# Kernel tuning notes

Hardware: AMD Instinct MI355X
Metric: run time of the kernel (lower is better)

Reference implementation:

```python
import jax, jax.numpy as jnp
import numpy as np

# Static configuration (matches init_kwargs)
B, C, H, W = 8, 64, 256, 256
WS = 8            # window size
HEADS = 4
DH = 16           # dim per head, HEADS*DH == C
L = WS * WS       # tokens per window
EPS_LN = 1e-5

# --- Swin relative-position index (static, numpy) ---
_coords = np.stack(np.meshgrid(np.arange(WS), np.arange(WS), indexing='ij'))  # [2,ws,ws]
_flat = _coords.reshape(2, -1)                                                # [2,L]
_rel = (_flat[:, :, None] - _flat[:, None, :]).transpose(1, 2, 0).copy()      # [L,L,2]
_rel[..., 0] += WS - 1
_rel[..., 1] += WS - 1
_rel[..., 0] *= 2 * WS - 1
REL_IDX = _rel.sum(-1)  # [L,L] ints in [0, (2ws-1)^2)


def _biasfree_ln(x, w):
    # x: [B,C,H,W]; BiasFree_LayerNorm over channel dim (biased var, no mean subtraction in scale)
    var = jnp.var(x, axis=1, keepdims=True)
    return x * jax.lax.rsqrt(var + EPS_LN) * w[None, :, None, None]


def _win_partition(t):  # [B,H,W,C] -> [N, L, C]
    t = t.reshape(B, H // WS, WS, W // WS, WS, C).transpose(0, 1, 3, 2, 4, 5)
    return t.reshape(-1, L, C)


def _win_reverse(t):  # [N, L, C] -> [B,H,W,C]
    t = t.reshape(B, H // WS, W // WS, WS, WS, C).transpose(0, 1, 3, 2, 4, 5)
    return t.reshape(B, H, W, C)


def _l2norm(t):
    # torch F.normalize(dim=-1) semantics
    n = jnp.sqrt(jnp.sum(t * t, axis=-1, keepdims=True))
    return t / jnp.maximum(n, 1e-12)


def _forward(x, illu_fea, ln1_w, ln2_w, w_qkv, b_qkv, rpb_table, w_proj, b_proj,
             temperature, w_qkv_m, w_dw, w_out_m):
    # ---------- spatial (window) attention branch ----------
    xs = _biasfree_ln(x, ln1_w).transpose(0, 2, 3, 1)          # [B,H,W,C]
    xw = _win_partition(xs)                                     # [N,L,C]
    iw = _win_partition(illu_fea.transpose(0, 2, 3, 1))         # [N,L,C]
    iw = iw.reshape(-1, L, HEADS, DH).transpose(0, 2, 1, 3)     # [N,h,L,d]

    qkv = (xw @ w_qkv + b_qkv).reshape(-1, L, 3, HEADS, DH).transpose(2, 0, 3, 1, 4)
    q, k, v = qkv[0], qkv[1], qkv[2]                            # [N,h,L,d]
    scale = DH ** (-0.5)
    attn = jnp.einsum('nhld,nhmd->nhlm', q * scale, k)          # [N,h,L,L]
    bias = rpb_table[REL_IDX.reshape(-1)].reshape(L, L, HEADS).transpose(2, 0, 1)
    attn = jax.nn.softmax(attn + bias[None], axis=-1)
    v = v * iw                                                  # illumination modulation
    out = jnp.einsum('nhlm,nhmd->nhld', attn, v)
    out = out.transpose(0, 2, 1, 3).reshape(-1, L, C) @ w_proj + b_proj
    win_out = _win_reverse(out).transpose(0, 3, 1, 2)           # [B,C,H,W]

    # ---------- channel (MDTA) attention branch ----------
    xm = _biasfree_ln(x, ln2_w)
    qkv_m = jnp.einsum('oc,bchw->bohw', w_qkv_m, xm)            # 1x1 conv, [B,3C,H,W]
    qkv_m = jax.lax.conv_general_dilated(
        qkv_m, w_dw, (1, 1), 'SAME', feature_group_count=3 * C,
        dimension_numbers=('NCHW', 'OIHW', 'NCHW'))             # depthwise 3x3
    qm, km, vm = jnp.split(qkv_m, 3, axis=1)                    # [B,C,H,W] each

    def heads(t):
        return t.reshape(B, HEADS, DH, H * W)                   # b (n d) h w -> b n d (hw)
    qm, km, vm, im = heads(qm), heads(km), heads(vm), heads(illu_fea)
    qm = _l2norm(qm)
    km = _l2norm(km)
    attn_c = jnp.einsum('bndx,bnex->bnde', qm, km) * temperature[None]  # [B,h,d,d]
    attn_c = jax.nn.softmax(attn_c, axis=-1)
    vm = vm * im                                                # illumination modulation
    out_c = jnp.einsum('bnde,bnex->bndx', attn_c, vm).reshape(B, C, H, W)
    mdta_out = jnp.einsum('oc,bchw->bohw', w_out_m, out_c)

    return x + win_out + mdta_out


def setup_inputs() -> dict:
    key = jax.random.key(0)
    ks = jax.random.split(key, 10)
    f32 = jnp.float32
    return {
        'x': jax.random.normal(ks[0], (B, C, H, W), f32),
        'illu_fea': jax.random.uniform(ks[1], (B, C, H, W), f32),
        'ln1_w': jnp.ones((C,), f32),
        'ln2_w': jnp.ones((C,), f32),
        'w_qkv': jax.random.normal(ks[2], (C, 3 * C), f32) * 0.02,
        'b_qkv': jnp.zeros((3 * C,), f32),
        'rpb_table': jax.random.normal(ks[3], ((2 * WS - 1) ** 2, HEADS), f32) * 0.02,
        'w_proj': jax.random.normal(ks[4], (C, C), f32) * 0.02,
        'b_proj': jnp.zeros((C,), f32),
        'temperature': jnp.ones((HEADS, 1, 1), f32),
        'w_qkv_m': jax.random.normal(ks[5], (3 * C, C), f32) * 0.02,
        'w_dw': jax.random.normal(ks[6], (3 * C, 1, 3, 3), f32) * 0.1,
        'w_out_m': jax.random.normal(ks[7], (C, C), f32) * 0.02,
    }


def reference(x, illu_fea, ln1_w, ln2_w, w_qkv, b_qkv, rpb_table, w_proj, b_proj,
              temperature, w_qkv_m, w_dw, w_out_m):
    return _forward(x, illu_fea, ln1_w, ln2_w, w_qkv, b_qkv, rpb_table, w_proj,
                    b_proj, temperature, w_qkv_m, w_dw, w_out_m)
```

## Files before the change

### kernel.cpp

```cpp
#include <hip/hip_runtime.h>
#include <hip/hip_bf16.h>

#define HW 65536
#define WIDTH 256
#define SP_OFF 77856768ull

typedef __attribute__((ext_vector_type(8))) short short8v;
typedef __attribute__((ext_vector_type(4))) short short4v;
typedef __attribute__((ext_vector_type(4))) float f32x4;

__device__ inline float bf2f(unsigned short u) {
  unsigned int i = ((unsigned int)u) << 16;
  float f; __builtin_memcpy(&f, &i, 4); return f;
}
__device__ inline unsigned short f2bf(float x) {
  __hip_bfloat16 h = __float2bfloat16(x);
  unsigned short u; __builtin_memcpy(&u, &h, 2); return u;
}

#define XH_IDX(p, g) ((p)*64 + ((((g) ^ ((p)&7)))<<3))
#define QC_IDX(ch, px) ((ch)*256 + ((((px)>>3) ^ ((ch)&7))<<3) + ((px)&7))
#define QCG_IDX(ch, G) ((ch)*256 + ((((G) ^ ((ch)&7)))<<3))

__global__ __launch_bounds__(256, 3) void k_spatial(
    const float* __restrict__ x, const float* __restrict__ illu,
    const float* __restrict__ ln1w, const float* __restrict__ wqkv,
    const float* __restrict__ bqkv, const float* __restrict__ rpb,
    const float* __restrict__ wproj, const float* __restrict__ bproj,
    float* __restrict__ out, unsigned short* __restrict__ sp, int use_sp)
{
  __shared__ __align__(16) unsigned short shbuf[9216];
  __shared__ __align__(16) unsigned short ks[64*72];
  __shared__ __align__(16) unsigned short vs[64*72];
  __shared__ __align__(16) unsigned short vsT[64*72];
  __shared__ float rpbs[900];
  __shared__ float rs_tok[64];

  unsigned short* xw = shbuf;
  unsigned short* qs = shbuf + 4608;

  const int tid = threadIdx.x;
  const int b = blockIdx.x & 7;
  const int grp = blockIdx.x >> 3;
  const float* xb = x + (size_t)b * 64 * HW;
  const float* ib = illu + (size_t)b * 64 * HW;

  const int lane = tid & 63;
  const int w = tid >> 6;
  const int fr = lane & 15;
  const int fg = lane >> 4;
  const int hb = w * 16;

  for (int i = tid; i < 900; i += 256) rpbs[i] = rpb[i];

  short8v bfq[3][2];
  float biasr[3];
  #pragma unroll
  for (int part = 0; part < 3; ++part) {
    int o = part * 64 + hb + fr;
    biasr[part] = bqkv[o];
    #pragma unroll
    for (int kh = 0; kh < 2; ++kh)
      #pragma unroll
      for (int j = 0; j < 8; ++j) {
        int c = kh * 32 + fg * 8 + j;
        bfq[part][kh][j] = (short)f2bf(wqkv[c * 192 + o] * ln1w[c]);
      }
  }
  short8v bfp[2];
  #pragma unroll
  for (int kh = 0; kh < 2; ++kh)
    #pragma unroll
    for (int j = 0; j < 8; ++j) {
      int c = kh * 32 + fg * 8 + j;
      bfp[kh][j] = (short)f2bf(wproj[c * 64 + hb + fr]);
    }

  for (int wi = 0; wi < 4; ++wi) {
    const int win = (grp << 2) + wi;
    const int h0 = (win >> 5) << 3;
    const int w0 = (win & 31) << 3;

    for (int i = tid; i < 1024; i += 256) {
      int c = i >> 4, seg = i & 15;
      int row = seg >> 1, half = (seg & 1) * 4;
      float4 v4 = *(const float4*)&xb[(size_t)c * HW + (h0 + row) * WIDTH + w0 + half];
      int p = row * 8 + half;
      xw[(p+0)*72 + c] = f2bf(v4.x);
      xw[(p+1)*72 + c] = f2bf(v4.y);
      xw[(p+2)*72 + c] = f2bf(v4.z);
      xw[(p+3)*72 + c] = f2bf(v4.w);
    }
    __syncthreads();
    {
      int l = tid >> 2, q4 = tid & 3;
      short8v v8a = *(const short8v*)&xw[l*72 + q4*16];
      short8v v8b = *(const short8v*)&xw[l*72 + q4*16 + 8];
      float s = 0.f, s2 = 0.f;
      #pragma unroll
      for (int j = 0; j < 8; ++j) {
        float va = bf2f((unsigned short)v8a[j]), vb = bf2f((unsigned short)v8b[j]);
        s += va + vb; s2 += va * va + vb * vb;
      }
      s += __shfl_down(s, 1); s2 += __shfl_down(s2, 1);
      s += __shfl_down(s, 2); s2 += __shfl_down(s2, 2);
      if (q4 == 0) {
        float mean = s * 0.015625f;
        float var = s2 * 0.015625f - mean * mean;
        rs_tok[l] = rsqrtf(var + 1e-5f);
      }
    }
    __syncthreads();
    {
      short8v a[4][2];
      #pragma unroll
      for (int rt = 0; rt < 4; ++rt)
        #pragma unroll
        for (int kh = 0; kh < 2; ++kh)
          a[rt][kh] = *(const short8v*)&xw[(rt*16 + fr)*72 + kh*32 + fg*8];
      #pragma unroll
      for (int part = 0; part < 3; ++part) {
        float bias = biasr[part];
        #pragma unroll
        for (int rt = 0; rt < 4; ++rt) {
          f32x4 acc = {0.f, 0.f, 0.f, 0.f};
          acc = __builtin_amdgcn_mfma_f32_16x16x32_bf16(a[rt][0], bfq[part][0], acc, 0, 0, 0);
          acc = __builtin_amdgcn_mfma_f32_16x16x32_bf16(a[rt][1], bfq[part][1], acc, 0, 0, 0);
          #pragma unroll
          for (int r = 0; r < 4; ++r) {
            int t = rt*16 + fg*4 + r;
            float val = acc[r] * rs_tok[t] + bias;
            if (part == 0)      qs[t*72 + hb + fr] = f2bf(val * 0.25f);
            else if (part == 1) ks[t*72 + hb + fr] = f2bf(val);
            else                vs[t*72 + hb + fr] = f2bf(val);
          }
        }
      }
    }
    __syncthreads();
    for (int i = tid; i < 1024; i += 256) {
      int c = i >> 4, seg = i & 15;
      int row = seg >> 1, half = (seg & 1) * 4;
      float4 v4 = *(const float4*)&ib[(size_t)c * HW + (h0 + row) * WIDTH + w0 + half];
      int p = row * 8 + half;
      xw[(p+0)*72 + c] = f2bf(v4.x);
      xw[(p+1)*72 + c] = f2bf(v4.y);
      xw[(p+2)*72 + c] = f2bf(v4.z);
      xw[(p+3)*72 + c] = f2bf(v4.w);
    }
    __syncthreads();
    for (int i = tid; i < 4096; i += 256) {
      int l = i >> 6, c = i & 63;
      unsigned short vb16 = f2bf(bf2f(vs[l*72 + c]) * bf2f(xw[l*72 + c]));
      vs[l*72 + c] = vb16;
      vsT[c*72 + ((((l >> 3) ^ (c & 7)) << 3) | (l & 7))] = vb16;
    }
    __syncthreads();
    float inv_s[4];
    {
      short8v zero8 = {0,0,0,0,0,0,0,0};
      short8v kf[4], qf[4];
      #pragma unroll
      for (int t = 0; t < 4; ++t) {
        if (fg < 2) {
          kf[t] = *(const short8v*)&ks[(t*16 + fr)*72 + hb + fg*8];
          qf[t] = *(const short8v*)&qs[(t*16 + fr)*72 + hb + fg*8];
        } else { kf[t] = zero8; qf[t] = zero8; }
      }
      f32x4 st[4][4];
      #pragma unroll
      for (int kt = 0; kt < 4; ++kt)
        #pragma unroll
        for (int qt = 0; qt < 4; ++qt) {
          f32x4 z = {0.f, 0.f, 0.f, 0.f};
          st[kt][qt] = __builtin_amdgcn_mfma_f32_16x16x32_bf16(kf[kt], qf[qt], z, 0, 0, 0);
        }
      float sc[4][16];
      #pragma unroll
      for (int qt = 0; qt < 4; ++qt) {
        int qi = qt*2 + (fr >> 3);
        int qj = fr & 7;
        float mx = -1e30f;
        #pragma unroll
        for (int kt = 0; kt < 4; ++kt) {
          int ki = kt*2 + (fg >> 1);
          int kj0 = (fg & 1) * 4;
          int base = ((qi - ki + 7)*15 + (qj - kj0 + 7))*4 + w;
          #pragma unroll
          for (int r = 0; r < 4; ++r) {
            float v = st[kt][qt][r] + rpbs[base - 4*r];
            sc[qt][kt*4 + r] = v;
            mx = fmaxf(mx, v);
          }
        }
        mx = fmaxf(mx, __shfl_xor(mx, 16));
        mx = fmaxf(mx, __shfl_xor(mx, 32));
        float ss = 0.f;
        #pragma unroll
        for (int j = 0; j < 16; ++j) { float e = __expf(sc[qt][j] - mx); sc[qt][j] = e; ss += e; }
        ss += __shfl_xor(ss, 16);
        ss += __shfl_xor(ss, 32);
        inv_s[qt] = 1.f / ss;
      }
      __syncthreads();
      unsigned short* pb = shbuf + w * 2304;
      f32x4 ot[4];
      #pragma unroll
      for (int nt = 0; nt < 4; ++nt) { f32x4 z = {0.f,0.f,0.f,0.f}; ot[nt] = z; }
      #pragma unroll
      for (int P = 0; P < 2; ++P) {
        #pragma unroll
        for (int qt = 0; qt < 4; ++qt)
          #pragma unroll
          for (int k2 = 0; k2 < 2; ++k2) {
            int kt = 2*P + k2;
            unsigned int lo = (unsigned)f2bf(sc[qt][kt*4+0]) | ((unsigned)f2bf(sc[qt][kt*4+1]) << 16);
            unsigned int hi = (unsigned)f2bf(sc[qt][kt*4+2]) | ((unsigned)f2bf(sc[qt][kt*4+3]) << 16);
            uint2 pk; pk.x = lo; pk.y = hi;
            *(uint2*)&pb[(qt*16 + fr)*36 + k2*16 + fg*4] = pk;
          }
        __syncthreads();
        short8v av = *(const short8v*)&vsT[(hb + fr)*72 + (((P*4 + fg) ^ ((hb + fr) & 7)) << 3)];
        #pragma unroll
        for (int nt = 0; nt < 4; ++nt) {
          short4v p0 = *(const short4v*)&pb[(nt*16 + fr)*36 + fg*8];
          short4v p1 = *(const short4v*)&pb[(nt*16 + fr)*36 + fg*8 + 4];
          short8v bv;
          #pragma unroll
          for (int j = 0; j < 4; ++j) { bv[j] = p0[j]; bv[4+j] = p1[j]; }
          ot[nt] = __builtin_amdgcn_mfma_f32_16x16x32_bf16(av, bv, ot[nt], 0, 0, 0);
        }
        __syncthreads();
      }
      #pragma unroll
      for (int nt = 0; nt < 4; ++nt) {
        float iv = inv_s[nt];
        unsigned int lo = (unsigned)f2bf(ot[nt][0]*iv) | ((unsigned)f2bf(ot[nt][1]*iv) << 16);
        unsigned int hi = (unsigned)f2bf(ot[nt][2]*iv) | ((unsigned)f2bf(ot[nt][3]*iv) << 16);
        uint2 pk; pk.x = lo; pk.y = hi;
        *(uint2*)&ks[(nt*16 + fr)*72 + hb + fg*4] = pk;
      }
    }
    __syncthreads();
    {
      short8v a[4][2];
      #pragma unroll
      for (int rt = 0; rt < 4; ++rt)
        #pragma unroll
        for (int kh = 0; kh < 2; ++kh)
          a[rt][kh] = *(const short8v*)&ks[(rt*16 + fr)*72 + kh*32 + fg*8];
      #pragma unroll
      for (int rt = 0; rt < 4; ++rt) {
        f32x4 acc = {0.f, 0.f, 0.f, 0.f};
        acc = __builtin_amdgcn_mfma_f32_16x16x32_bf16(a[rt][0], bfp[0], acc, 0, 0, 0);
        acc = __builtin_amdgcn_mfma_f32_16x16x32_bf16(a[rt][1], bfp[1], acc, 0, 0, 0);
        #pragma unroll
        for (int r = 0; r < 4; ++r)
          vs[(rt*16 + fg*4 + r)*72 + hb + fr] = f2bf(acc[r]);
      }
    }
    __syncthreads();
    if (use_sp) {
      unsigned short* spw = sp + (size_t)(b * 1024 + win) * 4096;
      for (int i = tid; i < 1024; i += 256) {
        int row = i >> 7, rem = i & 127;
        int c = rem >> 1, half = (rem & 1) * 4;
        int p = row * 8 + half;
        size_t gofs = (size_t)c * HW + (h0 + row) * WIDTH + w0 + half;
        float4 xr4 = *(const float4*)&xb[gofs];
        float bp = bproj[c];
        unsigned int lo = (unsigned)f2bf(xr4.x + bp + bf2f(vs[(p+0)*72 + c]))
                        | ((unsigned)f2bf(xr4.y + bp + bf2f(vs[(p+1)*72 + c])) << 16);
        unsigned int hi = (unsigned)f2bf(xr4.z + bp + bf2f(vs[(p+2)*72 + c]))
                        | ((unsigned)f2bf(xr4.w + bp + bf2f(vs[(p+3)*72 + c])) << 16);
        uint2 pk; pk.x = lo; pk.y = hi;
        *(uint2*)&spw[row*512 + c*8 + half] = pk;
      }
    } else {
      for (int i = tid; i < 1024; i += 256) {
        int o = i >> 4, seg = i & 15;
        int row = seg >> 1, half = (seg & 1) * 4;
        int p = row * 8 + half;
        size_t gofs = (size_t)o * HW + (h0 + row) * WIDTH + w0 + half;
        float4 xr4 = *(const float4*)&xb[gofs];
        float bp = bproj[o];
        float4 r;
        r.x = xr4.x + bp + bf2f(vs[(p+0)*72 + o]);
        r.y = xr4.y + bp + bf2f(vs[(p+1)*72 + o]);
        r.z = xr4.z + bp + bf2f(vs[(p+2)*72 + o]);
        r.w = xr4.w + bp + bf2f(vs[(p+3)*72 + o]);
        *(float4*)&out[(size_t)b * 64 * HW + gofs] = r;
      }
    }
    __syncthreads();
  }
}

__global__ __launch_bounds__(256, 2) void k_chan_qkv(
    const float* __restrict__ x, const float* __restrict__ illu,
    const float* __restrict__ ln2w, const float* __restrict__ w1,
    const float* __restrict__ wdw,
    unsigned short* __restrict__ vm, float* __restrict__ Gp,
    float* __restrict__ Nqp, float* __restrict__ Nkp)
{
  __shared__ __align__(16) unsigned short xh[324*64];
  __shared__ __align__(16) unsigned short tb[32*360];
  __shared__ __align__(16) unsigned short qc[16*256];
  __shared__ __align__(16) unsigned short kc[16*256];

  float* rsp = (float*)tb;

  const int tid = threadIdx.x;
  const int blk = ((blockIdx.x & 7) << 8) | (blockIdx.x >> 3);
  const int b = blk >> 8;
  const int tile = blk & 255;
  const int ty0 = (tile >> 4) << 4, tx0 = (tile & 15) << 4;
  const float* xb = x + (size_t)b * 64 * HW;

  for (int i = tid; i < 64 * 324; i += 256) {
    int c = i / 324, p = i - c * 324;
    int hy = p / 18, hx = p - hy * 18;
    int gy = ty0 + hy - 1, gx = tx0 + hx - 1;
    float v = 0.f;
    if (gy >= 0 && gy < 256 && gx >= 0 && gx < 256)
      v = xb[(size_t)c * HW + gy * WIDTH + gx];
    xh[XH_IDX(p, c >> 3) + (c & 7)] = f2bf(v);
  }
  __syncthreads();
  for (int p = tid; p < 324; p += 256) {
    float s = 0.f, s2 = 0.f;
    #pragma unroll
    for (int g = 0; g < 8; ++g) {
      short8v v8 = *(const short8v*)&xh[XH_IDX(p, g)];
      #pragma unroll
      for (int j = 0; j < 8; ++j) { float v = bf2f((unsigned short)v8[j]); s += v; s2 += v * v; }
    }
    float mean = s * 0.015625f;
    float var = s2 * 0.015625f - mean * mean;
    rsp[p] = rsqrtf(var + 1e-5f);
  }
  __syncthreads();
  for (int i = tid; i < 2592; i += 256) {
    int p = i >> 3;
    float rs = rsp[p];
    short8v v8 = *(const short8v*)&xh[i * 8];
    #pragma unroll
    for (int j = 0; j < 8; ++j) v8[j] = (short)f2bf(bf2f((unsigned short)v8[j]) * rs);
    *(short8v*)&xh[i * 8] = v8;
  }
  __syncthreads();

  const int lane = tid & 63;
  const int wid = tid >> 6;
  const int fcol = lane & 15;
  const int fk = lane >> 4;
  const int dpy = (tid >> 2) & 15;
  const int dg = tid & 3;

  auto gemm32 = [&](int qb, int kb) {
    short8v bq[2], bk[2];
    const float* wrq = w1 + (size_t)(qb + fcol) * 64;
    const float* wrk = w1 + (size_t)(kb + fcol) * 64;
    #pragma unroll
    for (int s = 0; s < 2; ++s) {
      int cs = fk * 8 + s * 32;
      #pragma unroll
      for (int j = 0; j < 8; ++j) {
        float lw = ln2w[cs + j];
        bq[s][j] = (short)f2bf(wrq[cs + j] * lw);
        bk[s][j] = (short)f2bf(wrk[cs + j] * lw);
      }
    }
    for (int t = wid; t < 21; t += 4) {
      int ar = t * 16 + fcol;
      short8v a0, a1;
      if (ar < 324) {
        a0 = *(const short8v*)&xh[XH_IDX(ar, fk)];
        a1 = *(const short8v*)&xh[XH_IDX(ar, fk + 4)];
      } else {
        short8v z = {0,0,0,0,0,0,0,0};
        a0 = z; a1 = z;
      }
      f32x4 aq = {0.f, 0.f, 0.f, 0.f};
      f32x4 ak = {0.f, 0.f, 0.f, 0.f};
      aq = __builtin_amdgcn_mfma_f32_16x16x32_bf16(a0, bq[0], aq, 0, 0, 0);
      aq = __builtin_amdgcn_mfma_f32_16x16x32_bf16(a1, bq[1], aq, 0, 0, 0);
      ak = __builtin_amdgcn_mfma_f32_16x16x32_bf16(a0, bk[0], ak, 0, 0, 0);
      ak = __builtin_amdgcn_mfma_f32_16x16x32_bf16(a1, bk[1], ak, 0, 0, 0);
      #pragma unroll
      for (int r = 0; r < 4; ++r) {
        int px = t * 16 + fk * 4 + r;
        if (px < 324) {
          int hy = px / 18, hx = px - hy * 18;
          tb[fcol * 360 + hy * 20 + hx]        = f2bf(aq[r]);
          tb[(16 + fcol) * 360 + hy * 20 + hx] = f2bf(ak[r]);
        }
      }
    }
  };

  float dout8[8][4];
  auto dw32 = [&](int qwb, int kwb) {
    #pragma unroll
    for (int oc8 = 0; oc8 < 8; ++oc8) {
      int oc = wid * 8 + oc8;
      int ch = (oc < 16) ? (qwb + oc) : (kwb + oc - 16);
      const float* w9 = wdw + (size_t)ch * 9;
      float wk[9];
      #pragma unroll
      for (int t = 0; t < 9; ++t) wk[t] = w9[t];
      float a0 = 0.f, a1 = 0.f, a2 = 0.f, a3 = 0.f;
      #pragma unroll
      for (int ky = 0; ky < 3; ++ky) {
        int base = oc * 360 + (dpy + ky) * 20 + dg * 4;
        short4v t4 = *(const short4v*)&tb[base];
        unsigned int t2 = *(const unsigned int*)&tb[base + 4];
        float e0 = bf2f((unsigned short)t4[0]);
        float e1 = bf2f((unsigned short)t4[1]);
        float e2 = bf2f((unsigned short)t4[2]);
        float e3 = bf2f((unsigned short)t4[3]);
        float e4 = bf2f((unsigned short)(t2 & 0xffff));
        float e5 = bf2f((unsigned short)(t2 >> 16));
        float k0 = wk[ky*3+0], k1 = wk[ky*3+1], k2 = wk[ky*3+2];
        a0 += k0*e0 + k1*e1 + k2*e2;
        a1 += k0*e1 + k1*e2 + k2*e3;
        a2 += k0*e2 + k1*e3 + k2*e4;
        a3 += k0*e3 + k1*e4 + k2*e5;
      }
      dout8[oc8][0] = a0; dout8[oc8][1] = a1;
      dout8[oc8][2] = a2; dout8[oc8][3] = a3;
    }
  };

  for (int n = 0; n < 4; ++n) {
    gemm32(16 * n, 64 + 16 * n);
    __syncthreads();
    dw32(16 * n, 64 + 16 * n);
    #pragma unroll
    for (int oc8 = 0; oc8 < 8; ++oc8) {
      int oc = wid * 8 + oc8;
      unsigned short* dst = (oc < 16) ? qc : kc;
      int row = oc & 15;
      #pragma unroll
      for (int i = 0; i < 4; ++i)
        dst[QC_IDX(row, dpy*16 + dg*4 + i)] = f2bf(dout8[oc8][i]);
    }
    __syncthreads();
    {
      int ch = tid >> 4, seg = tid & 15;
      float sq = 0.f, sk = 0.f;
      #pragma unroll
      for (int j = 0; j < 16; ++j) {
        float vq = bf2f(qc[QC_IDX(ch, seg * 16 + j)]); sq += vq * vq;
        float vk = bf2f(kc[QC_IDX(ch, seg * 16 + j)]); sk += vk * vk;
      }
      sq += __shfl_xor(sq, 1); sq += __shfl_xor(sq, 2); sq += __shfl_xor(sq, 4); sq += __shfl_xor(sq, 8);
      sk += __shfl_xor(sk, 1); sk += __shfl_xor(sk, 2); sk += __shfl_xor(sk, 4); sk += __shfl_xor(sk, 8);
      if (seg == 0) {
        Nqp[(size_t)blk * 64 + n * 16 + ch] = sq;
        Nkp[(size_t)blk * 64 + n * 16 + ch] = sk;
      }
    }
    if (wid == 0) {
      f32x4 g = {0.f, 0.f, 0.f, 0.f};
      #pragma unroll
      for (int s = 0; s < 8; ++s) {
        int G = fk + 4 * s;
        short8v aq = *(const short8v*)&qc[QCG_IDX(fcol, G)];
        short8v bk = *(const short8v*)&kc[QCG_IDX(fcol, G)];
        g = __builtin_amdgcn_mfma_f32_16x16x32_bf16(aq, bk, g, 0, 0, 0);
      }
      float* gp = Gp + ((size_t)blk * 4 + n) * 256;
      #pragma unroll
      for (int r = 0; r < 4; ++r) gp[(fk * 4 + r) * 16 + fcol] = g[r];
    }
  }
  const float* ib = illu + (size_t)b * 64 * HW;
  for (int j = 0; j < 2; ++j) {
    gemm32(128 + 32 * j, 144 + 32 * j);
    __syncthreads();
    dw32(128 + 32 * j, 144 + 32 * j);
    int gy = ty0 + dpy, gx = tx0 + dg * 4;
    size_t ppos = (size_t)gy * WIDTH + gx;
    #pragma unroll
    for (int oc8 = 0; oc8 < 8; ++oc8) {
      int vc = 32 * j + wid * 8 + oc8;
      float4 iv4 = *(const float4*)&ib[(size_t)vc * HW + ppos];
      unsigned int lo = (unsigned)f2bf(dout8[oc8][0] * iv4.x)
                      | ((unsigned)f2bf(dout8[oc8][1] * iv4.y) << 16);
      unsigned int hi = (unsigned)f2bf(dout8[oc8][2] * iv4.z)
                      | ((unsigned)f2bf(dout8[oc8][3] * iv4.w) << 16);
      uint2 pk; pk.x = lo; pk.y = hi;
      *(uint2*)&vm[((size_t)b * 64 + vc) * HW + ppos] = pk;
    }
    __syncthreads();
  }
}

__global__ __launch_bounds__(256) void k_reduce1(
    const float* __restrict__ Gp, const float* __restrict__ Nqp, const float* __restrict__ Nkp,
    float* __restrict__ G2, float* __restrict__ Nq2, float* __restrict__ Nk2)
{
  const int blk = blockIdx.x;
  const int b = blk >> 5, g = blk & 31;
  const int tid = threadIdx.x;
  float ga[4] = {0.f, 0.f, 0.f, 0.f};
  for (int t = 0; t < 8; ++t) {
    const float* src = Gp + ((size_t)(b * 256 + g * 8 + t)) * 1024;
    #pragma unroll
    for (int j = 0; j < 4; ++j) ga[j] += src[tid + j * 256];
  }
  float* dst = G2 + ((size_t)(b * 32 + g)) * 1024;
  #pragma unroll
  for (int j = 0; j < 4; ++j) dst[tid + j * 256] = ga[j];
  if (tid < 128) {
    int ch = tid & 63; bool isq = tid < 64;
    const float* np = isq ? Nqp : Nkp;
    float s = 0.f;
    for (int t = 0; t < 8; ++t) s += np[((size_t)(b * 256 + g * 8 + t)) * 64 + ch];
    (isq ? Nq2 : Nk2)[(size_t)(b * 32 + g) * 64 + ch] = s;
  }
}

__global__ __launch_bounds__(256) void k_reduce2(
    const float* __restrict__ G2, const float* __restrict__ Nq2, const float* __restrict__ Nk2,
    const float* __restrict__ temp, const float* __restrict__ wout, float* __restrict__ M)
{
  __shared__ float Gs[1024];
  __shared__ float As[4][16][17];
  __shared__ float nq[64], nk[64];
  const int b = blockIdx.x;
  const int tid = threadIdx.x;
  float ga[4] = {0.f, 0.f, 0.f, 0.f};
  for (int g = 0; g < 32; ++g) {
    const float* src = G2 + ((size_t)(b * 32 + g)) * 1024;
    #pragma unroll
    for (int j = 0; j < 4; ++j) ga[j] += src[tid + j * 256];
  }
  #pragma unroll
  for (int j = 0; j < 4; ++j) Gs[tid + j * 256] = ga[j];
  if (tid < 128) {
    int ch = tid & 63; bool isq = tid < 64;
    const float* n2 = isq ? Nq2 : Nk2;
    float s = 0.f;
    for (int g = 0; g < 32; ++g) s += n2[(size_t)(b * 32 + g) * 64 + ch];
    float r = fmaxf(sqrtf(s), 1e-12f);
    (isq ? nq : nk)[ch] = r;
  }
  __syncthreads();
  if (tid < 64) {
    int n = tid >> 4, d = tid & 15;
    float tv = temp[n];
    float row[16]; float mx = -1e30f;
    #pragma unroll
    for (int e = 0; e < 16; ++e) {
      float v = Gs[n * 256 + d * 16 + e] / (nq[n * 16 + d] * nk[n * 16 + e]) * tv;
      row[e] = v; mx = fmaxf(mx, v);
    }
    float s = 0.f;
    #pragma unroll
    for (int e = 0; e < 16; ++e) { float ev = __expf(row[e] - mx); row[e] = ev; s += ev; }
    float inv = 1.f / s;
    #pragma unroll
    for (int e = 0; e < 16; ++e) As[n][d][e] = row[e] * inv;
  }
  __syncthreads();
  float* Mb = M + (size_t)b * 4096;
  for (int i = tid; i < 4096; i += 256) {
    int o = i >> 6, cp = i & 63;
    int n = cp >> 4, e = cp & 15;
    float a = 0.f;
    #pragma unroll
    for (int d = 0; d < 16; ++d) a += wout[o * 64 + n * 16 + d] * As[n][d][e];
    Mb[i] = a;
  }
}

__global__ __launch_bounds__(256, 3) void k_mdta_out(
    const unsigned short* __restrict__ vm, const float* __restrict__ M,
    const unsigned short* __restrict__ sp, int use_sp,
    float* __restrict__ out)
{
  __shared__ __align__(16) float Ml[4096];
  __shared__ __align__(16) unsigned short spl[64 * 264];
  const int blk = blockIdx.x;
  const int b = blk >> 8;
  const int y = blk & 255;
  const int tid = threadIdx.x;

  const float* Mb = M + (size_t)b * 4096;
  for (int i = tid; i < 4096; i += 256) Ml[i] = Mb[i];
  if (use_sp) {
    int wy = y >> 3, py = y & 7;
    const unsigned short* spb = sp + ((((size_t)b * 1024 + wy * 32) * 8) + py) * 512;
    for (int k = 0; k < 8; ++k) {
      int i3 = k * 256 + tid;
      int o = i3 & 63, wx = i3 >> 6;
      short8v v8 = *(const short8v*)&spb[(size_t)wx * 4096 + o * 8];
      *(short8v*)&spl[o * 264 + wx * 8] = v8;
    }
  }
  __syncthreads();
  float xcol[64];
  const unsigned short* vb = vm + (size_t)b * 64 * HW + y * 256 + tid;
  #pragma unroll
  for (int c = 0; c < 64; ++c) xcol[c] = bf2f(vb[(size_t)c * HW]);
  float* ob = out + (size_t)b * 64 * HW + y * 256 + tid;
  for (int o = 0; o < 64; ++o) {
    const float4* mr = (const float4*)&Ml[o * 64];
    float acc = 0.f;
    #pragma unroll
    for (int g = 0; g < 16; ++g) {
      float4 m4 = mr[g];
      acc += m4.x * xcol[g*4] + m4.y * xcol[g*4+1] + m4.z * xcol[g*4+2] + m4.w * xcol[g*4+3];
    }
    if (use_sp) ob[(size_t)o * HW] = bf2f(spl[o * 264 + tid]) + acc;
    else        ob[(size_t)o * HW] += acc;
  }
}

extern "C" void kernel_launch(void* const* d_in, const int* in_sizes, int n_in,
                              void* d_out, int out_size, void* d_ws, size_t ws_size,
                              hipStream_t stream) {
  const float* x     = (const float*)d_in[0];
  const float* illu  = (const float*)d_in[1];
  const float* ln1w  = (const float*)d_in[2];
  const float* ln2w  = (const float*)d_in[3];
  const float* wqkv  = (const float*)d_in[4];
  const float* bqkv  = (const float*)d_in[5];
  const float* rpb   = (const float*)d_in[6];
  const float* wproj = (const float*)d_in[7];
  const float* bproj = (const float*)d_in[8];
  const float* temp  = (const float*)d_in[9];
  const float* w1    = (const float*)d_in[10];
  const float* wdw   = (const float*)d_in[11];
  const float* wout  = (const float*)d_in[12];
  float* out = (float*)d_out;

  char* ws = (char*)d_ws;
  unsigned short* vm = (unsigned short*)ws;
  float* Gp  = (float*)(ws + 67108864);
  float* Nqp = (float*)(ws + 75497472);
  float* Nkp = (float*)(ws + 76021760);
  float* G2  = (float*)(ws + 76546048);
  float* Nq2 = (float*)(ws + 77594624);
  float* Nk2 = (float*)(ws + 77660160);
  float* M   = (float*)(ws + 77725696);
  unsigned short* sp = (unsigned short*)(ws + SP_OFF);
  int use_sp = (ws_size >= SP_OFF + 67108864ull) ? 1 : 0;

  k_spatial<<<2048, 256, 0, stream>>>(x, illu, ln1w, wqkv, bqkv, rpb, wproj, bproj,
                                      out, sp, use_sp);
  k_chan_qkv<<<2048, 256, 0, stream>>>(x, illu, ln2w, w1, wdw, vm, Gp, Nqp, Nkp);
  k_reduce1<<<256, 256, 0, stream>>>(Gp, Nqp, Nkp, G2, Nq2, Nk2);
  k_reduce2<<<8, 256, 0, stream>>>(G2, Nq2, Nk2, temp, wout, M);
  k_mdta_out<<<2048, 256, 0, stream>>>(vm, M, sp, use_sp, out);
}
```

Before: 725.2 us.

## Merge spatial and channel-QKV kernels into one launch with interleaved blocks

Folds the spatial window-attention kernel and the channel QKV/depthwise kernel into a single kernel, with even blocks running the spatial body and odd blocks the channel body over one shared-memory buffer. Both branches read the same x/illu tiles at about the same time, so the goal is cache sharing, overlap of two different workloads on the CUs, and one fewer launch and tail. The cost is that every block reserves the larger shared-memory footprint (about 79KB) and the spatial work drops to two blocks per CU from three, which lowers its occupancy.

```diff
diff --git a/kernel.cpp b/kernel.cpp
--- a/kernel.cpp
+++ b/kernel.cpp
@@ -22,26 +22,27 @@
 #define QC_IDX(ch, px) ((ch)*256 + ((((px)>>3) ^ ((ch)&7))<<3) + ((px)&7))
 #define QCG_IDX(ch, G) ((ch)*256 + ((((G) ^ ((ch)&7)))<<3))
 
-__global__ __launch_bounds__(256, 3) void k_spatial(
+__device__ __forceinline__ void spatial_body(
+    unsigned char* smem, int sub,
     const float* __restrict__ x, const float* __restrict__ illu,
     const float* __restrict__ ln1w, const float* __restrict__ wqkv,
     const float* __restrict__ bqkv, const float* __restrict__ rpb,
     const float* __restrict__ wproj, const float* __restrict__ bproj,
     float* __restrict__ out, unsigned short* __restrict__ sp, int use_sp)
 {
-  __shared__ __align__(16) unsigned short shbuf[9216];
-  __shared__ __align__(16) unsigned short ks[64*72];
-  __shared__ __align__(16) unsigned short vs[64*72];
-  __shared__ __align__(16) unsigned short vsT[64*72];
-  __shared__ float rpbs[900];
-  __shared__ float rs_tok[64];
+  unsigned short* shbuf = (unsigned short*)smem;
+  unsigned short* ks    = (unsigned short*)(smem + 18432);
+  unsigned short* vs    = (unsigned short*)(smem + 27648);
+  unsigned short* vsT   = (unsigned short*)(smem + 36864);
+  float* rpbs           = (float*)(smem + 46080);
+  float* rs_tok         = (float*)(smem + 49680);
 
   unsigned short* xw = shbuf;
   unsigned short* qs = shbuf + 4608;
 
   const int tid = threadIdx.x;
-  const int b = blockIdx.x & 7;
-  const int grp = blockIdx.x >> 3;
+  const int b = sub & 7;
+  const int grp = sub >> 3;
   const float* xb = x + (size_t)b * 64 * HW;
   const float* ib = illu + (size_t)b * 64 * HW;
 
@@ -296,22 +297,22 @@
   }
 }
 
-__global__ __launch_bounds__(256, 2) void k_chan_qkv(
+__device__ __forceinline__ void chan_body(
+    unsigned char* smem, int sub,
     const float* __restrict__ x, const float* __restrict__ illu,
     const float* __restrict__ ln2w, const float* __restrict__ w1,
     const float* __restrict__ wdw,
     unsigned short* __restrict__ vm, float* __restrict__ Gp,
     float* __restrict__ Nqp, float* __restrict__ Nkp)
 {
-  __shared__ __align__(16) unsigned short xh[324*64];
-  __shared__ __align__(16) unsigned short tb[32*360];
-  __shared__ __align__(16) unsigned short qc[16*256];
-  __shared__ __align__(16) unsigned short kc[16*256];
-
+  unsigned short* xh = (unsigned short*)smem;
+  unsigned short* tb = (unsigned short*)(smem + 41472);
+  unsigned short* qc = (unsigned short*)(smem + 64512);
+  unsigned short* kc = (unsigned short*)(smem + 72704);
   float* rsp = (float*)tb;
 
   const int tid = threadIdx.x;
-  const int blk = ((blockIdx.x & 7) << 8) | (blockIdx.x >> 3);
+  const int blk = ((sub & 7) << 8) | (sub >> 3);
   const int b = blk >> 8;
   const int tile = blk & 255;
   const int ty0 = (tile >> 4) << 4, tx0 = (tile & 15) << 4;
@@ -495,6 +496,25 @@
     }
     __syncthreads();
   }
+}
+
+__global__ __launch_bounds__(256, 2) void k_fused(
+    const float* __restrict__ x, const float* __restrict__ illu,
+    const float* __restrict__ ln1w, const float* __restrict__ ln2w,
+    const float* __restrict__ wqkv, const float* __restrict__ bqkv,
+    const float* __restrict__ rpb, const float* __restrict__ wproj,
+    const float* __restrict__ bproj, const float* __restrict__ w1,
+    const float* __restrict__ wdw,
+    float* __restrict__ out, unsigned short* __restrict__ sp, int use_sp,
+    unsigned short* __restrict__ vm, float* __restrict__ Gp,
+    float* __restrict__ Nqp, float* __restrict__ Nkp)
+{
+  __shared__ __align__(16) unsigned char smem[80896];
+  const int sub = blockIdx.x >> 1;
+  if (blockIdx.x & 1)
+    chan_body(smem, sub, x, illu, ln2w, w1, wdw, vm, Gp, Nqp, Nkp);
+  else
+    spatial_body(smem, sub, x, illu, ln1w, wqkv, bqkv, rpb, wproj, bproj, out, sp, use_sp);
 }
 
 __global__ __launch_bounds__(256) void k_reduce1(
@@ -649,9 +669,8 @@
   unsigned short* sp = (unsigned short*)(ws + SP_OFF);
   int use_sp = (ws_size >= SP_OFF + 67108864ull) ? 1 : 0;
 
-  k_spatial<<<2048, 256, 0, stream>>>(x, illu, ln1w, wqkv, bqkv, rpb, wproj, bproj,
-                                      out, sp, use_sp);
-  k_chan_qkv<<<2048, 256, 0, stream>>>(x, illu, ln2w, w1, wdw, vm, Gp, Nqp, Nkp);
+  k_fused<<<4096, 256, 0, stream>>>(x, illu, ln1w, ln2w, wqkv, bqkv, rpb, wproj, bproj,
+                                    w1, wdw, out, sp, use_sp, vm, Gp, Nqp, Nkp);
   k_reduce1<<<256, 256, 0, stream>>>(Gp, Nqp, Nkp, G2, Nq2, Nk2);
   k_reduce2<<<8, 256, 0, stream>>>(G2, Nq2, Nk2, temp, wout, M);
   k_mdta_out<<<2048, 256, 0, stream>>>(vm, M, sp, use_sp, out);
```

Result: faster. 655.6 us (-9.6%).
